# Optimization experiments

Measured on AMD Instinct MI355X. Metric: run time of the kernel, lower is better.

The kernel has to match this reference:

```python
import jax, jax.numpy as jnp
import numpy as np

P = 5  # patch_size from init_kwargs


def _unfold(x, p):
    """torch.nn.functional.unfold equivalent for a [1,C,H,W] image.
    Returns [L, C*p*p] (already squeezed + transposed, matching the module).
    Feature ordering is channel-major then kernel row-major, same as torch."""
    C, H, W = x.shape[1], x.shape[2], x.shape[3]
    h, w = H - p + 1, W - p + 1
    # [C, p*p, h, w] -> [C*p*p, h*w] -> [L, C*p*p]
    patches = jnp.stack([x[0, :, i:i + h, j:j + w]
                         for i in range(p) for j in range(p)], axis=1)
    return patches.reshape(C * p * p, h * w).T


def setup_inputs() -> dict:
    key = jax.random.key(0)
    k1, k2 = jax.random.split(key)
    crop = jax.random.normal(k1, (1, 3, 128, 128), dtype=jnp.float32)
    original_image = jax.random.normal(k2, (1, 3, 128, 128), dtype=jnp.float32)
    return {"crop": crop, "original_image": original_image}


def reference(crop, original_image):
    X = _unfold(crop, P)            # [n, k] crop patches
    Y = _unfold(original_image, P)  # [m, k] original patches (precomputed in __init__)
    # calc_dist_l2: X2 - 2*X@Y^T + Y2  -> [n, m]
    X2 = jnp.sum(X * X, axis=1, keepdims=True)   # [n, 1]
    Y2 = jnp.sum(Y * Y, axis=1)[None, :]         # [1, m]
    dists = X2 - 2.0 * (X @ Y.T) + Y2            # [n, m]
    nn_dists = jnp.min(dists, axis=1)            # [n]
    nn_idx = jnp.argmin(dists, axis=1)           # [n] int
    loss = jnp.mean(nn_dists)
    return (loss, nn_idx)
```

## Files before the change

kernel.cpp:

```cpp
#include <hip/hip_runtime.h>
#include <hip/hip_bf16.h>

#define NPATCH 15376
#define NP     15488
#define NT     121
#define ATILES 128
#define TILE_SHORTS 12288
#define EPSA   1.75f
#define PMSTR  16384

typedef __attribute__((ext_vector_type(8))) __bf16 bf16x8;
typedef __attribute__((ext_vector_type(4))) float  f32x4;
typedef __attribute__((ext_vector_type(4))) _Float16 f16x4;
typedef float __attribute__((ext_vector_type(4), aligned(4))) f32x4u;

__device__ __forceinline__ unsigned short f2bf(float x) {
    __hip_bfloat16 h = __float2bfloat16(x);
    return *(unsigned short*)&h;
}
__device__ __forceinline__ float bf2f(unsigned short u) {
    __hip_bfloat16 h; *(unsigned short*)&h = u;
    return __bfloat162float(h);
}
__device__ __forceinline__ unsigned int fsort(float d) {
    unsigned int b = __builtin_bit_cast(unsigned int, d);
    return (b & 0x80000000u) ? ~b : (b | 0x80000000u);
}

__device__ __forceinline__ float patch_sq(const float* __restrict__ img, int p) {
    int pr = p / 124, pc = p - pr * 124;
    const float* base = img + pr * 128 + pc;
    float s = 0.f;
    #pragma unroll
    for (int ch = 0; ch < 3; ++ch)
        #pragma unroll
        for (int di = 0; di < 5; ++di)
            #pragma unroll
            for (int dj = 0; dj < 5; ++dj) {
                float v = base[ch * 16384 + di * 128 + dj];
                s = fmaf(v, v, s);
            }
    return s;
}
__global__ void sqnorm2(const float* __restrict__ crop, const float* __restrict__ orig,
                        float* __restrict__ X2, float* __restrict__ Y2,
                        unsigned int* __restrict__ WLn, unsigned long long* __restrict__ RES) {
    int p = blockIdx.x * 256 + threadIdx.x;
    if (p == 0) *WLn = 0;
    if (p < NP) {
        Y2[p] = (p < NPATCH) ? patch_sq(orig, p) : 3.0e38f;
    } else {
        int q = p - NP;
        if (q < NPATCH) { X2[q] = patch_sq(crop, q); RES[q] = 0xFFFFFFFFFFFFFFFFULL; }
    }
}

__global__ void pack2(const float* __restrict__ crop, const float* __restrict__ orig,
                      unsigned short* __restrict__ Abig, unsigned short* __restrict__ Bbig,
                      const float* __restrict__ Y2) {
    int cid = blockIdx.x * 256 + threadIdx.x;
    const float* img;
    unsigned short* dst;
    bool isA;
    if (cid < ATILES * 1536) { img = crop; dst = Abig; isA = true; }
    else { cid -= ATILES * 1536; img = orig; dst = Bbig; isA = false; }
    int t = cid / 1536, rem = cid - t * 1536;
    int s = rem >> 7, r = rem & 127;
    int row = t * 128 + r;
    unsigned short ch8[8];
    #pragma unroll
    for (int e = 0; e < 8; ++e) {
        int k = s * 8 + e;
        unsigned short v = 0;
        if (k < 75) {
            if (row < NPATCH) {
                int c = k / 25, rem2 = k - c * 25;
                int di = rem2 / 5, dj = rem2 - di * 5;
                int pr = row / 124, pc = row - pr * 124;
                v = f2bf(img[c * 16384 + (pr + di) * 128 + (pc + dj)]);
            }
        } else if (k < 77) {
            if (isA) v = f2bf(-0.5f);
            else {
                float yv = Y2[row];
                unsigned short hi = f2bf(yv);
                v = (k == 75) ? hi : f2bf(yv - bf2f(hi));
            }
        }
        ch8[e] = v;
    }
    *(ulonglong2*)(dst + (size_t)cid * 8) = *(ulonglong2*)ch8;
}

__global__ __launch_bounds__(256, 2)
void dist_mfma6(const unsigned short* __restrict__ A, const unsigned short* __restrict__ B,
                _Float16* __restrict__ PMh) {
    __shared__ _Float16 stash[4][16][64];

    const int tid = threadIdx.x, lane = tid & 63, wid = tid >> 6;
    const int l15 = lane & 15, l4 = lane >> 4;

    const int g = blockIdx.x * 4 + wid;
    const int cg = g & 1;
    const int chunk = (g >> 1) & 7;
    const int rowgroup = g >> 4;
    const int t0 = chunk * 15 + (chunk ? 1 : 0);
    const int nt = chunk ? 15 : 16;

    bf16x8 a[4][3];
    {
        const int atile = rowgroup >> 1, rbase = (rowgroup & 1) * 64;
        const unsigned short* Ab =
            A + ((size_t)atile * 12 + l4) * 1024 + (size_t)(rbase + l15) * 8;
        #pragma unroll
        for (int mi = 0; mi < 4; ++mi)
            #pragma unroll
            for (int k3 = 0; k3 < 3; ++k3)
                a[mi][k3] = *(const bf16x8*)(Ab + k3 * 4096 + mi * 128);
    }

    const size_t cgofs = (size_t)cg * 512 + (size_t)l15 * 8;
    bf16x8 b0[12], b1[12];

#define BLOAD(bank, tile)                                                         \
    {                                                                             \
        const unsigned short* _B = B + ((size_t)(tile) * 12 + l4) * 1024 + cgofs; \
        _Pragma("unroll")                                                         \
        for (int _ni = 0; _ni < 4; ++_ni)                                         \
            _Pragma("unroll")                                                     \
            for (int _k3 = 0; _k3 < 3; ++_k3)                                     \
                bank[_ni * 3 + _k3] = *(const bf16x8*)(_B + _k3 * 4096 + _ni * 128); \
    }

#define COMPUTE(bank, it)                                                         \
    {                                                                             \
        f32x4 acc[4][4];                                                          \
        _Pragma("unroll")                                                         \
        for (int _k3 = 0; _k3 < 3; ++_k3)                                         \
            _Pragma("unroll")                                                     \
            for (int _mi = 0; _mi < 4; ++_mi)                                     \
                _Pragma("unroll")                                                 \
                for (int _ni = 0; _ni < 4; ++_ni)                                 \
                    acc[_mi][_ni] = __builtin_amdgcn_mfma_f32_16x16x32_bf16(      \
                        bank[_ni * 3 + _k3], a[_mi][_k3],                         \
                        (_k3 == 0) ? (f32x4){0.f, 0.f, 0.f, 0.f} : acc[_mi][_ni], \
                        0, 0, 0);                                                 \
        _Pragma("unroll")                                                         \
        for (int _mi = 0; _mi < 4; ++_mi) {                                       \
            float _m = acc[_mi][0][0];                                            \
            _Pragma("unroll")                                                     \
            for (int _ni = 0; _ni < 4; ++_ni)                                     \
                _Pragma("unroll")                                                 \
                for (int _j = 0; _j < 4; ++_j)                                    \
                    if (_ni + _j) _m = fmaxf(_m, acc[_mi][_ni][_j]);              \
            _m = fmaxf(_m, __shfl_xor(_m, 16));                                   \
            _m = fmaxf(_m, __shfl_xor(_m, 32));                                   \
            if (l4 == 0) stash[wid][it][_mi * 16 + l15] = (_Float16)_m;           \
        }                                                                         \
    }

    BLOAD(b0, t0);
    int it = 0;
    while (true) {
        if (it + 1 < nt) BLOAD(b1, t0 + it + 1);
        COMPUTE(b0, it);
        ++it;
        if (it >= nt) break;
        if (it + 1 < nt) BLOAD(b0, t0 + it + 1);
        COMPUTE(b1, it);
        ++it;
        if (it >= nt) break;
    }
#undef BLOAD
#undef COMPUTE

    for (int i2 = 0; i2 < nt; ++i2)
        PMh[(size_t)((t0 + i2) * 2 + cg) * PMSTR + rowgroup * 64 + lane] = stash[wid][i2][lane];
}

__global__ __launch_bounds__(256)
void flag_kernel(const _Float16* __restrict__ PMh,
                 unsigned int* __restrict__ WL, unsigned int* __restrict__ WLn) {
    __shared__ _Float16 cachev[NT][256];
    __shared__ int scan[256];
    __shared__ unsigned int sbase;

    const int tid = threadIdx.x;
    const int r = blockIdx.x * 256 + tid;
    const int rr = (r < NPATCH) ? r : (NPATCH - 1);

    float mt = -3.4e38f;
    for (int t = 0; t < NT; ++t) {
        float v0 = (float)PMh[(size_t)(2 * t) * PMSTR + rr];
        float v1 = (float)PMh[(size_t)(2 * t + 1) * PMSTR + rr];
        float v = fmaxf(v0, v1);
        cachev[t][tid] = (_Float16)v;
        mt = fmaxf(mt, v);
    }
    const float thr = mt - EPSA;

    int cnt = 0;
    if (r < NPATCH)
        for (int t = 0; t < NT; ++t)
            cnt += ((float)cachev[t][tid] >= thr) ? 1 : 0;

    scan[tid] = cnt;
    __syncthreads();
    for (int s = 1; s < 256; s <<= 1) {
        int v = (tid >= s) ? scan[tid - s] : 0;
        __syncthreads();
        scan[tid] += v;
        __syncthreads();
    }
    if (tid == 255) sbase = atomicAdd(WLn, (unsigned int)scan[255]);
    __syncthreads();

    if (r < NPATCH) {
        unsigned int w = sbase + (unsigned int)(scan[tid] - cnt);
        for (int t = 0; t < NT; ++t)
            if ((float)cachev[t][tid] >= thr)
                WL[w++] = ((unsigned int)r << 7) | (unsigned int)t;
    }
}

__global__ __launch_bounds__(256)
void repair_items(const float* __restrict__ crop, const float* __restrict__ orig,
                  const float* __restrict__ X2, const float* __restrict__ Y2,
                  const unsigned int* __restrict__ WL, const unsigned int* __restrict__ WLn,
                  unsigned long long* __restrict__ RES) {
    const int lane = threadIdx.x & 63;
    const unsigned int gw = (blockIdx.x * 256 + threadIdx.x) >> 6;
    const unsigned int nw = (gridDim.x * 256) >> 6;
    const unsigned int n = *WLn;

    for (unsigned int i = gw; i < n; i += nw) {
        const unsigned int item = __builtin_amdgcn_readfirstlane(WL[i]);
        const int r = (int)(item >> 7), tile = (int)(item & 127u);
        const int pr = r / 124, pc = r - pr * 124;
        const float* xb = crop + pr * 128 + pc;
        const float x2 = X2[r];

        unsigned long long best = 0xFFFFFFFFFFFFFFFFULL;
        #pragma unroll
        for (int h = 0; h < 2; ++h) {
            const int j = tile * 128 + h * 64 + lane;
            if (j < NPATCH) {
                const int jr = j / 124, jc = j - jr * 124;
                const float* yb = orig + jr * 128 + jc;
                float dot = 0.f;
                #pragma unroll
                for (int ch = 0; ch < 3; ++ch) {
                    const float* ybc = yb + ch * 16384;
                    const float* xbc = xb + ch * 16384;
                    #pragma unroll
                    for (int di = 0; di < 5; ++di) {
                        const f32x4u y4 = *(const f32x4u*)(ybc + di * 128);
                        const float  y1 = ybc[di * 128 + 4];
                        dot = fmaf(xbc[di * 128 + 0], y4.x, dot);
                        dot = fmaf(xbc[di * 128 + 1], y4.y, dot);
                        dot = fmaf(xbc[di * 128 + 2], y4.z, dot);
                        dot = fmaf(xbc[di * 128 + 3], y4.w, dot);
                        dot = fmaf(xbc[di * 128 + 4], y1,  dot);
                    }
                }
                float d = fmaf(-2.f, dot, x2) + Y2[j];
                unsigned long long k = (((unsigned long long)fsort(d)) << 32) | (unsigned int)j;
                if (k < best) best = k;
            }
        }
        #pragma unroll
        for (int off = 1; off < 64; off <<= 1) {
            unsigned long long o = __shfl_xor(best, off);
            if (o < best) best = o;
        }
        if (lane == 0) atomicMin(RES + r, best);
    }
}

__global__ void finalize_kernel(const unsigned long long* __restrict__ RES,
                                float* __restrict__ out, float* __restrict__ rsum) {
    int r = blockIdx.x * 256 + threadIdx.x;
    if (r >= NPATCH) return;
    unsigned long long v = RES[r];
    unsigned int j = (unsigned int)v;
    unsigned int u = (unsigned int)(v >> 32);
    unsigned int b = (u & 0x80000000u) ? (u ^ 0x80000000u) : ~u;
    out[1 + r] = (float)j;
    rsum[r] = __builtin_bit_cast(float, b);
}

__global__ void loss_final(const float* __restrict__ rsum, float* __restrict__ out) {
    __shared__ float s[256];
    float acc = 0.f;
    for (int i = threadIdx.x; i < NPATCH; i += 256) acc += rsum[i];
    s[threadIdx.x] = acc;
    __syncthreads();
    for (int st = 128; st > 0; st >>= 1) {
        if (threadIdx.x < st) s[threadIdx.x] += s[threadIdx.x + st];
        __syncthreads();
    }
    if (threadIdx.x == 0) out[0] = s[0] / (float)NPATCH;
}

extern "C" void kernel_launch(void* const* d_in, const int* in_sizes, int n_in,
                              void* d_out, int out_size, void* d_ws, size_t ws_size,
                              hipStream_t stream) {
    const float* crop = (const float*)d_in[0];
    const float* orig = (const float*)d_in[1];
    float* out = (float*)d_out;

    unsigned short* Abig = (unsigned short*)d_ws;
    unsigned short* Bbig = Abig + (size_t)ATILES * TILE_SHORTS;
    _Float16* PMh = (_Float16*)(Bbig + (size_t)NT * TILE_SHORTS);
    float* X2 = (float*)(PMh + (size_t)242 * PMSTR);
    float* Y2 = X2 + NPATCH;
    unsigned long long* RES = (unsigned long long*)(Y2 + NP);
    float* RS = (float*)(RES + NPATCH);
    unsigned int* WLn = (unsigned int*)(RS + NPATCH);
    unsigned int* WL = WLn + 16;

    sqnorm2<<<(NP + NPATCH + 255) / 256, 256, 0, stream>>>(crop, orig, X2, Y2, WLn, RES);
    pack2<<<(ATILES + NT) * 6, 256, 0, stream>>>(crop, orig, Abig, Bbig, Y2);
    dist_mfma6<<<1024, 256, 0, stream>>>(Abig, Bbig, PMh);
    flag_kernel<<<(NPATCH + 255) / 256, 256, 0, stream>>>(PMh, WL, WLn);
    repair_items<<<2048, 256, 0, stream>>>(crop, orig, X2, Y2, WL, WLn, RES);
    finalize_kernel<<<(NPATCH + 255) / 256, 256, 0, stream>>>(RES, out, RS);
    loss_final<<<1, 256, 0, stream>>>(RS, out);
}
```

Before: 159.6 us.

## Retune candidate threshold, split MFMA work finer, batch repair items per wave

The approximate-search margin EPSA is tightened, so fewer candidate tiles are flagged for exact fp32 repair. The MFMA distance kernel splits the column tiles into 16 groups instead of 8 and launches twice as many blocks, giving more parallelism. The flag kernel uses single-wave blocks with a shuffle scan instead of a shared-memory scan, and it now also does the RES initialisation. The repair kernel processes four work items per wave to raise memory-level parallelism and amortise the reductions. The risk is that the smaller margin lets a wrong nearest neighbour slip through the bf16 prefilter.

```diff
diff --git a/kernel.cpp b/kernel.cpp
--- a/kernel.cpp
+++ b/kernel.cpp
@@ -2,11 +2,10 @@
 #include <hip/hip_bf16.h>
 
 #define NPATCH 15376
-#define NP     15488
 #define NT     121
 #define ATILES 128
 #define TILE_SHORTS 12288
-#define EPSA   1.75f
+#define EPSA   1.30f
 #define PMSTR  16384
 
 typedef __attribute__((ext_vector_type(8))) __bf16 bf16x8;
@@ -27,32 +26,37 @@
     return (b & 0x80000000u) ? ~b : (b | 0x80000000u);
 }
 
-__device__ __forceinline__ float patch_sq(const float* __restrict__ img, int p) {
-    int pr = p / 124, pc = p - pr * 124;
+__global__ void sqnorm2(const float* __restrict__ crop, const float* __restrict__ orig,
+                        float* __restrict__ X2, float* __restrict__ Y2,
+                        unsigned int* __restrict__ WLn) {
+    int p = blockIdx.x * 256 + threadIdx.x;
+    if (p == 0) *WLn = 0;
+    const float* img;
+    float* dst;
+    int q;
+    if (p < NPATCH) { img = orig; dst = Y2; q = p; }
+    else {
+        q = p - NPATCH;
+        if (q >= NPATCH) return;
+        img = crop; dst = X2;
+    }
+    int pr = q / 124, pc = q - pr * 124;
     const float* base = img + pr * 128 + pc;
     float s = 0.f;
     #pragma unroll
     for (int ch = 0; ch < 3; ++ch)
         #pragma unroll
-        for (int di = 0; di < 5; ++di)
-            #pragma unroll
-            for (int dj = 0; dj < 5; ++dj) {
-                float v = base[ch * 16384 + di * 128 + dj];
-                s = fmaf(v, v, s);
-            }
-    return s;
-}
-__global__ void sqnorm2(const float* __restrict__ crop, const float* __restrict__ orig,
-                        float* __restrict__ X2, float* __restrict__ Y2,
-                        unsigned int* __restrict__ WLn, unsigned long long* __restrict__ RES) {
-    int p = blockIdx.x * 256 + threadIdx.x;
-    if (p == 0) *WLn = 0;
-    if (p < NP) {
-        Y2[p] = (p < NPATCH) ? patch_sq(orig, p) : 3.0e38f;
-    } else {
-        int q = p - NP;
-        if (q < NPATCH) { X2[q] = patch_sq(crop, q); RES[q] = 0xFFFFFFFFFFFFFFFFULL; }
-    }
+        for (int di = 0; di < 5; ++di) {
+            const int o = ch * 16384 + di * 128;
+            const f32x4u v = *(const f32x4u*)(base + o);
+            const float  w = base[o + 4];
+            s = fmaf(v.x, v.x, s);
+            s = fmaf(v.y, v.y, s);
+            s = fmaf(v.z, v.z, s);
+            s = fmaf(v.w, v.w, s);
+            s = fmaf(w,  w,  s);
+        }
+    dst[q] = s;
 }
 
 __global__ void pack2(const float* __restrict__ crop, const float* __restrict__ orig,
@@ -82,7 +86,7 @@
         } else if (k < 77) {
             if (isA) v = f2bf(-0.5f);
             else {
-                float yv = Y2[row];
+                float yv = (row < NPATCH) ? Y2[row] : 3.0e38f;
                 unsigned short hi = f2bf(yv);
                 v = (k == 75) ? hi : f2bf(yv - bf2f(hi));
             }
@@ -95,17 +99,17 @@
 __global__ __launch_bounds__(256, 2)
 void dist_mfma6(const unsigned short* __restrict__ A, const unsigned short* __restrict__ B,
                 _Float16* __restrict__ PMh) {
-    __shared__ _Float16 stash[4][16][64];
+    __shared__ _Float16 stash[4][8][64];
 
     const int tid = threadIdx.x, lane = tid & 63, wid = tid >> 6;
     const int l15 = lane & 15, l4 = lane >> 4;
 
     const int g = blockIdx.x * 4 + wid;
     const int cg = g & 1;
-    const int chunk = (g >> 1) & 7;
-    const int rowgroup = g >> 4;
-    const int t0 = chunk * 15 + (chunk ? 1 : 0);
-    const int nt = chunk ? 15 : 16;
+    const int cgrp = (g >> 1) & 15;
+    const int rowgroup = g >> 5;
+    const int t0 = (cgrp < 9) ? cgrp * 8 : 72 + (cgrp - 9) * 7;
+    const int nt = (cgrp < 9) ? 8 : 7;
 
     bf16x8 a[4][3];
     {
@@ -178,15 +182,14 @@
         PMh[(size_t)((t0 + i2) * 2 + cg) * PMSTR + rowgroup * 64 + lane] = stash[wid][i2][lane];
 }
 
-__global__ __launch_bounds__(256)
+__global__ __launch_bounds__(64)
 void flag_kernel(const _Float16* __restrict__ PMh,
-                 unsigned int* __restrict__ WL, unsigned int* __restrict__ WLn) {
-    __shared__ _Float16 cachev[NT][256];
-    __shared__ int scan[256];
-    __shared__ unsigned int sbase;
-
-    const int tid = threadIdx.x;
-    const int r = blockIdx.x * 256 + tid;
+                 unsigned int* __restrict__ WL, unsigned int* __restrict__ WLn,
+                 unsigned long long* __restrict__ RES) {
+    __shared__ _Float16 cachev[NT][64];
+
+    const int lane = threadIdx.x;
+    const int r = blockIdx.x * 64 + lane;
     const int rr = (r < NPATCH) ? r : (NPATCH - 1);
 
     float mt = -3.4e38f;
@@ -194,31 +197,32 @@
         float v0 = (float)PMh[(size_t)(2 * t) * PMSTR + rr];
         float v1 = (float)PMh[(size_t)(2 * t + 1) * PMSTR + rr];
         float v = fmaxf(v0, v1);
-        cachev[t][tid] = (_Float16)v;
+        cachev[t][lane] = (_Float16)v;
         mt = fmaxf(mt, v);
     }
+    if (r < NPATCH) RES[r] = 0xFFFFFFFFFFFFFFFFULL;
     const float thr = mt - EPSA;
 
     int cnt = 0;
     if (r < NPATCH)
         for (int t = 0; t < NT; ++t)
-            cnt += ((float)cachev[t][tid] >= thr) ? 1 : 0;
-
-    scan[tid] = cnt;
-    __syncthreads();
-    for (int s = 1; s < 256; s <<= 1) {
-        int v = (tid >= s) ? scan[tid - s] : 0;
-        __syncthreads();
-        scan[tid] += v;
-        __syncthreads();
-    }
-    if (tid == 255) sbase = atomicAdd(WLn, (unsigned int)scan[255]);
-    __syncthreads();
+            cnt += ((float)cachev[t][lane] >= thr) ? 1 : 0;
+
+    int sc = cnt;
+    #pragma unroll
+    for (int off = 1; off < 64; off <<= 1) {
+        int v = __shfl_up(sc, off);
+        if (lane >= off) sc += v;
+    }
+    unsigned int total = (unsigned int)__shfl(sc, 63);
+    unsigned int base = 0;
+    if (lane == 63) base = atomicAdd(WLn, total);
+    base = __shfl(base, 63);
 
     if (r < NPATCH) {
-        unsigned int w = sbase + (unsigned int)(scan[tid] - cnt);
+        unsigned int w = base + (unsigned int)(sc - cnt);
         for (int t = 0; t < NT; ++t)
-            if ((float)cachev[t][tid] >= thr)
+            if ((float)cachev[t][lane] >= thr)
                 WL[w++] = ((unsigned int)r << 7) | (unsigned int)t;
     }
 }
@@ -233,47 +237,102 @@
     const unsigned int nw = (gridDim.x * 256) >> 6;
     const unsigned int n = *WLn;
 
-    for (unsigned int i = gw; i < n; i += nw) {
-        const unsigned int item = __builtin_amdgcn_readfirstlane(WL[i]);
-        const int r = (int)(item >> 7), tile = (int)(item & 127u);
-        const int pr = r / 124, pc = r - pr * 124;
-        const float* xb = crop + pr * 128 + pc;
-        const float x2 = X2[r];
-
-        unsigned long long best = 0xFFFFFFFFFFFFFFFFULL;
-        #pragma unroll
-        for (int h = 0; h < 2; ++h) {
-            const int j = tile * 128 + h * 64 + lane;
-            if (j < NPATCH) {
-                const int jr = j / 124, jc = j - jr * 124;
-                const float* yb = orig + jr * 128 + jc;
-                float dot = 0.f;
+    for (unsigned int p = gw; 4 * p < n; p += nw) {
+        int r4[4], tl4[4];
+        const float* xb4[4];
+        float x24[4];
+        #pragma unroll
+        for (int k = 0; k < 4; ++k) {
+            unsigned int ii = 4 * p + k;
+            ii = (ii < n) ? ii : (n - 1);
+            const unsigned int item = __builtin_amdgcn_readfirstlane(WL[ii]);
+            r4[k] = (int)(item >> 7);
+            tl4[k] = (int)(item & 127u);
+            const int pr = r4[k] / 124, pc = r4[k] - pr * 124;
+            xb4[k] = crop + pr * 128 + pc;
+            x24[k] = X2[r4[k]];
+        }
+
+        int jj[4][2];
+        const float* yy[4][2];
+        float dd[4][2];
+        #pragma unroll
+        for (int k = 0; k < 4; ++k)
+            #pragma unroll
+            for (int h = 0; h < 2; ++h) {
+                jj[k][h] = min(tl4[k] * 128 + h * 64 + lane, NPATCH - 1);
+                yy[k][h] = orig + (jj[k][h] / 124) * 128 + (jj[k][h] % 124);
+                dd[k][h] = 0.f;
+            }
+
+        #pragma unroll
+        for (int ch = 0; ch < 3; ++ch) {
+            #pragma unroll
+            for (int di = 0; di < 5; ++di) {
+                const int o = ch * 16384 + di * 128;
+                f32x4u v[4][2];
+                float  w[4][2];
                 #pragma unroll
-                for (int ch = 0; ch < 3; ++ch) {
-                    const float* ybc = yb + ch * 16384;
-                    const float* xbc = xb + ch * 16384;
+                for (int k = 0; k < 4; ++k)
                     #pragma unroll
-                    for (int di = 0; di < 5; ++di) {
-                        const f32x4u y4 = *(const f32x4u*)(ybc + di * 128);
-                        const float  y1 = ybc[di * 128 + 4];
-                        dot = fmaf(xbc[di * 128 + 0], y4.x, dot);
-                        dot = fmaf(xbc[di * 128 + 1], y4.y, dot);
-                        dot = fmaf(xbc[di * 128 + 2], y4.z, dot);
-                        dot = fmaf(xbc[di * 128 + 3], y4.w, dot);
-                        dot = fmaf(xbc[di * 128 + 4], y1,  dot);
+                    for (int h = 0; h < 2; ++h) {
+                        v[k][h] = *(const f32x4u*)(yy[k][h] + o);
+                        w[k][h] = yy[k][h][o + 4];
                     }
-                }
-                float d = fmaf(-2.f, dot, x2) + Y2[j];
-                unsigned long long k = (((unsigned long long)fsort(d)) << 32) | (unsigned int)j;
-                if (k < best) best = k;
+                float xt[4][5];
+                #pragma unroll
+                for (int k = 0; k < 4; ++k)
+                    #pragma unroll
+                    for (int tp = 0; tp < 5; ++tp)
+                        xt[k][tp] = xb4[k][o + tp];
+                #pragma unroll
+                for (int tp = 0; tp < 4; ++tp)
+                    #pragma unroll
+                    for (int k = 0; k < 4; ++k)
+                        #pragma unroll
+                        for (int h = 0; h < 2; ++h)
+                            dd[k][h] = fmaf(xt[k][tp], v[k][h][tp], dd[k][h]);
+                #pragma unroll
+                for (int k = 0; k < 4; ++k)
+                    #pragma unroll
+                    for (int h = 0; h < 2; ++h)
+                        dd[k][h] = fmaf(xt[k][4], w[k][h], dd[k][h]);
             }
         }
-        #pragma unroll
-        for (int off = 1; off < 64; off <<= 1) {
-            unsigned long long o = __shfl_xor(best, off);
-            if (o < best) best = o;
-        }
-        if (lane == 0) atomicMin(RES + r, best);
+
+        float bd[4];
+        int   bj[4];
+        #pragma unroll
+        for (int k = 0; k < 4; ++k) {
+            const float e0 = fmaf(-2.f, dd[k][0], x24[k]) + Y2[jj[k][0]];
+            const float e1 = fmaf(-2.f, dd[k][1], x24[k]) + Y2[jj[k][1]];
+            const bool s = (e1 < e0) || (e1 == e0 && jj[k][1] < jj[k][0]);
+            bd[k] = s ? e1 : e0;
+            bj[k] = s ? jj[k][1] : jj[k][0];
+        }
+
+        float dm[4] = {bd[0], bd[1], bd[2], bd[3]};
+        #pragma unroll
+        for (int off = 1; off < 64; off <<= 1)
+            #pragma unroll
+            for (int k = 0; k < 4; ++k)
+                dm[k] = fminf(dm[k], __shfl_xor(dm[k], off));
+        int jc[4];
+        #pragma unroll
+        for (int k = 0; k < 4; ++k)
+            jc[k] = (bd[k] == dm[k]) ? bj[k] : 0x7fffffff;
+        #pragma unroll
+        for (int off = 1; off < 64; off <<= 1)
+            #pragma unroll
+            for (int k = 0; k < 4; ++k)
+                jc[k] = min(jc[k], __shfl_xor(jc[k], off));
+
+        if (lane == 0) {
+            #pragma unroll
+            for (int k = 0; k < 4; ++k)
+                atomicMin(RES + r4[k],
+                          (((unsigned long long)fsort(dm[k])) << 32) | (unsigned int)jc[k]);
+        }
     }
 }
 
@@ -314,15 +373,15 @@
     _Float16* PMh = (_Float16*)(Bbig + (size_t)NT * TILE_SHORTS);
     float* X2 = (float*)(PMh + (size_t)242 * PMSTR);
     float* Y2 = X2 + NPATCH;
-    unsigned long long* RES = (unsigned long long*)(Y2 + NP);
+    unsigned long long* RES = (unsigned long long*)(Y2 + NPATCH);
     float* RS = (float*)(RES + NPATCH);
     unsigned int* WLn = (unsigned int*)(RS + NPATCH);
     unsigned int* WL = WLn + 16;
 
-    sqnorm2<<<(NP + NPATCH + 255) / 256, 256, 0, stream>>>(crop, orig, X2, Y2, WLn, RES);
+    sqnorm2<<<(2 * NPATCH + 255) / 256, 256, 0, stream>>>(crop, orig, X2, Y2, WLn);
     pack2<<<(ATILES + NT) * 6, 256, 0, stream>>>(crop, orig, Abig, Bbig, Y2);
-    dist_mfma6<<<1024, 256, 0, stream>>>(Abig, Bbig, PMh);
-    flag_kernel<<<(NPATCH + 255) / 256, 256, 0, stream>>>(PMh, WL, WLn);
+    dist_mfma6<<<2048, 256, 0, stream>>>(Abig, Bbig, PMh);
+    flag_kernel<<<(NPATCH + 63) / 64, 64, 0, stream>>>(PMh, WL, WLn, RES);
     repair_items<<<2048, 256, 0, stream>>>(crop, orig, X2, Y2, WL, WLn, RES);
     finalize_kernel<<<(NPATCH + 255) / 256, 256, 0, stream>>>(RES, out, RS);
     loss_final<<<1, 256, 0, stream>>>(RS, out);
```

New measurement: 145.8 us. 1.09x faster.
